# Optimization experiments

Measured on AMD Instinct MI355X. Metric: run time of the kernel, lower is better.

Reference implementation:

```python
import jax, jax.numpy as jnp
import numpy as np

HIDDEN = 256
DEPTH = 6
N_MOLS = 5000
ATOMS_PER_MOL = 30
N_ATOMS = N_MOLS * ATOMS_PER_MOL  # 150000 real atoms (+1 padding row)
N_BONDS = 320000                  # directed bonds (+1 padding row)
MAX_NB = 6
ATOM_FDIM = 133
BOND_FDIM = 147


def setup_inputs() -> dict:
    key = jax.random.key(0)
    ks = jax.random.split(key, 8)
    # row 0 of every per-atom / per-bond array is the chemprop zero-padding row
    f_atoms = jax.random.normal(ks[0], (N_ATOMS + 1, ATOM_FDIM), jnp.float32).at[0].set(0.0)
    f_bonds = jax.random.normal(ks[1], (N_BONDS + 1, BOND_FDIM), jnp.float32).at[0].set(0.0)
    a2b = jax.random.randint(ks[2], (N_ATOMS + 1, MAX_NB), 0, N_BONDS + 1, dtype=jnp.int32).at[0].set(0)
    b2a = jax.random.randint(ks[3], (N_BONDS + 1,), 1, N_ATOMS + 1, dtype=jnp.int32).at[0].set(0)
    # directed bonds come in reverse pairs: bond 2k+1 <-> bond 2k+2 (index 0 = pad)
    ids = np.arange(1, N_BONDS + 1)
    rev = ids + np.where(ids % 2 == 1, 1, -1)
    b2revb = jnp.asarray(np.concatenate([[0], rev]), dtype=jnp.int32)
    # contiguous a_scope: molecule i owns atoms [1 + 30*i, 1 + 30*(i+1))
    mol_ids = jnp.repeat(jnp.arange(N_MOLS, dtype=jnp.int32), ATOMS_PER_MOL)
    s = 0.1
    W_i = (jax.random.normal(ks[4], (HIDDEN, BOND_FDIM), jnp.float32) * s)
    W_h = (jax.random.normal(ks[5], (HIDDEN, HIDDEN), jnp.float32) * s)
    W_o = (jax.random.normal(ks[6], (HIDDEN, ATOM_FDIM + HIDDEN), jnp.float32) * s)
    b_o = (jax.random.normal(ks[7], (HIDDEN,), jnp.float32) * s)
    return {"f_atoms": f_atoms, "f_bonds": f_bonds, "a2b": a2b, "b2a": b2a,
            "b2revb": b2revb, "mol_ids": mol_ids,
            "W_i": W_i, "W_h": W_h, "W_o": W_o, "b_o": b_o}


def reference(f_atoms, f_bonds, a2b, b2a, b2revb, mol_ids, W_i, W_h, W_o, b_o):
    # input = W_i(f_bonds) (no bias); message = act(input)
    inp = f_bonds @ W_i.T                       # [B+1, H]
    message = jax.nn.relu(inp)
    for _ in range(DEPTH - 1):
        # gather incoming bond messages per atom, sum over padded neighbor dim
        a_message = message[a2b].sum(axis=1)    # [A+1, H]
        # directed message update: sum at source atom minus reverse message
        message = a_message[b2a] - message[b2revb]  # [B+1, H]
        message = jax.nn.relu(inp + message @ W_h.T)  # dropout p=0 -> identity
    # readout per atom
    a_message = message[a2b].sum(axis=1)        # [A+1, H]
    a_input = jnp.concatenate([f_atoms, a_message], axis=1)  # [A+1, F_a+H]
    atom_hiddens = jax.nn.relu(a_input @ W_o.T + b_o)        # [A+1, H]
    # mean aggregation over each molecule's atoms (a_scope, contiguous, size 30)
    sums = jax.ops.segment_sum(atom_hiddens[1:], mol_ids, num_segments=N_MOLS)
    return sums / float(ATOMS_PER_MOL)
```

## Files before the change

### kernel.cpp

```cpp
#include <hip/hip_runtime.h>
#include <stdint.h>

#define HIDDEN 256
#define NMOLS 5000
#define APM 30
#define NATOMS 150000
#define NBONDS 320000
#define MAXNB 6
#define AFD 133
#define BFD 147
#define A1 (NATOMS + 1)
#define B1 (NBONDS + 1)
#define KI 160
#define KIP 168
#define KO 416

typedef __bf16 bfx8 __attribute__((ext_vector_type(8)));
typedef float fx4 __attribute__((ext_vector_type(4)));
typedef unsigned short u16x8 __attribute__((ext_vector_type(8)));
typedef unsigned int u32x4 __attribute__((ext_vector_type(4)));

__device__ __forceinline__ float b2f(unsigned short u) {
    union { unsigned int i; float f; } v; v.i = ((unsigned int)u) << 16; return v.f;
}
__device__ __forceinline__ unsigned short f2b(float f) {
    union { float f; unsigned int i; } v; v.f = f;
    unsigned int r = v.i + 0x7FFFu + ((v.i >> 16) & 1u);
    return (unsigned short)(r >> 16);
}
__device__ __forceinline__ void gload_lds16(const void* g, void* l) {
    __builtin_amdgcn_global_load_lds(
        (const __attribute__((address_space(1))) unsigned int*)g,
        (__attribute__((address_space(3))) unsigned int*)l, 16, 0, 0);
}

__global__ void k_convw(const float* __restrict__ Wi, const float* __restrict__ Wh,
                        const float* __restrict__ Wo,
                        unsigned short* __restrict__ wi, unsigned short* __restrict__ wh,
                        unsigned short* __restrict__ wo) {
    int t = blockIdx.x * 256 + threadIdx.x;
    if (t < 256 * KI) {
        int n = t / KI, k = t % KI;
        wi[t] = (k < BFD) ? f2b(Wi[n * BFD + k]) : (unsigned short)0;
        return;
    }
    int t2 = t - 256 * KI;
    if (t2 < 256 * 256) {
        wh[t2] = f2b(Wh[t2]);
        return;
    }
    int t3 = t2 - 256 * 256;
    if (t3 < 256 * KO) {
        int n = t3 / KO, k = t3 % KO;
        float v = 0.f;
        if (k < AFD) v = Wo[n * (AFD + HIDDEN) + k];
        else if (k >= 160) v = Wo[n * (AFD + HIDDEN) + AFD + (k - 160)];
        wo[t3] = f2b(v);
    }
}

__global__ __launch_bounds__(256) void k_gemm_wi(
    const float* __restrict__ fb, const unsigned short* __restrict__ wi,
    unsigned short* __restrict__ inp, unsigned short* __restrict__ msg0)
{
    __shared__ float s_f32[64 * BFD];
    __shared__ unsigned short s_bf[64 * KIP];
    const int m0 = blockIdx.x * 64;
    const int tid = threadIdx.x;

    {
        const size_t base = (size_t)m0 * BFD;
        const size_t tot = (size_t)B1 * BFD;
        const float4* src4 = (const float4*)(fb + base);
#pragma unroll
        for (int i = 0; i < 10; ++i) {
            const int t4 = i * 256 + tid;
            if (t4 < (64 * BFD) / 4) {
                const size_t f = base + (size_t)t4 * 4;
                float4 v;
                if (f + 4 <= tot) {
                    v = src4[t4];
                } else {
                    v.x = (f + 0 < tot) ? fb[f + 0] : 0.f;
                    v.y = (f + 1 < tot) ? fb[f + 1] : 0.f;
                    v.z = (f + 2 < tot) ? fb[f + 2] : 0.f;
                    v.w = (f + 3 < tot) ? fb[f + 3] : 0.f;
                }
                *(float4*)(s_f32 + t4 * 4) = v;
            }
        }
    }
    __syncthreads();

    {
        const int r = tid >> 2, p = tid & 3;
        const float* srow = s_f32 + r * BFD;
        unsigned short* drow = s_bf + r * KIP;
#pragma unroll
        for (int i = 0; i < 5; ++i) {
            const int c0 = (i * 4 + p) * 8;
            u16x8 o;
#pragma unroll
            for (int e = 0; e < 8; ++e) {
                float v = (c0 + e < BFD) ? srow[c0 + e] : 0.f;
                o[e] = f2b(v);
            }
            *(u16x8*)(drow + c0) = o;
        }
    }
    __syncthreads();

    const int wv = tid >> 6, ln = tid & 63;
    const int l15 = ln & 15, lhi = ln >> 4;
    fx4 acc[4][4];
#pragma unroll
    for (int a = 0; a < 4; ++a)
#pragma unroll
        for (int b = 0; b < 4; ++b)
#pragma unroll
            for (int q = 0; q < 4; ++q) acc[a][b][q] = 0.f;

#pragma unroll
    for (int ks = 0; ks < 5; ++ks) {
        const int kk = ks * 32 + lhi * 8;
        bfx8 af[4], bb[4];
#pragma unroll
        for (int mf = 0; mf < 4; ++mf) {
            const int rr = mf * 16 + l15;
            af[mf] = *(const bfx8*)(s_bf + rr * KIP + kk);
        }
#pragma unroll
        for (int nf = 0; nf < 4; ++nf) {
            const int n = wv * 64 + nf * 16 + l15;
            bb[nf] = *(const bfx8*)(wi + n * KI + kk);
        }
#pragma unroll
        for (int mf = 0; mf < 4; ++mf)
#pragma unroll
            for (int nf = 0; nf < 4; ++nf)
                acc[mf][nf] = __builtin_amdgcn_mfma_f32_16x16x32_bf16(af[mf], bb[nf], acc[mf][nf], 0, 0, 0);
    }

    __syncthreads();
    unsigned short* cbuf = (unsigned short*)s_f32;
    {
        const int cb = wv * 64 + l15;
        const int rb = lhi * 4;
#pragma unroll
        for (int mf = 0; mf < 4; ++mf)
#pragma unroll
            for (int j = 0; j < 4; ++j) {
                const int row = mf * 16 + rb + j;
#pragma unroll
                for (int nf = 0; nf < 4; ++nf) {
                    const int col = cb + nf * 16;
                    const int byte = (row * 512) + (((col * 2) & ~15) ^ ((row & 7) << 4)) + ((col * 2) & 15);
                    *(unsigned short*)((char*)cbuf + byte) = f2b(acc[mf][nf][j]);
                }
            }
    }
    __syncthreads();
#pragma unroll
    for (int i = 0; i < 8; ++i) {
        const int row = i * 8 + (tid >> 5);
        const int col16 = tid & 31;
        const int byte = row * 512 + ((col16 * 16) ^ ((row & 7) << 4));
        u16x8 c = *(const u16x8*)((const char*)cbuf + byte);
        const int g = m0 + row;
        if (g < B1) {
            u16x8 m;
#pragma unroll
            for (int e = 0; e < 8; ++e) m[e] = (c[e] & 0x8000u) ? (unsigned short)0 : c[e];
            *(u16x8*)(inp + (size_t)g * HIDDEN + col16 * 8) = c;
            *(u16x8*)(msg0 + (size_t)g * HIDDEN + col16 * 8) = m;
        }
    }
}

__global__ __launch_bounds__(256) void k_gemm_z(
    const unsigned short* __restrict__ msg,
    const unsigned short* __restrict__ wh,
    unsigned short* __restrict__ Z)
{
    __shared__ unsigned short lds[64 * 256];
    const int m0 = blockIdx.x * 64;
    const int tid = threadIdx.x;
    const int wv = tid >> 6, ln = tid & 63;

    {
        const int l2 = ln >> 5;
        const int q = (ln & 31) * 16;
#pragma unroll
        for (int r = 0; r < 8; ++r) {
            const int row = wv * 16 + r * 2 + l2;
            const size_t srcb = (size_t)(m0 + row) * 512 + (size_t)(q ^ ((row & 7) << 4));
            char* dst = (char*)lds + wv * 8192 + r * 1024;
            gload_lds16((const char*)msg + srcb, dst);
        }
    }
    __syncthreads();

    const int l15 = ln & 15, lhi = ln >> 4;
    fx4 acc[4][4];
#pragma unroll
    for (int a = 0; a < 4; ++a)
#pragma unroll
        for (int b = 0; b < 4; ++b)
#pragma unroll
            for (int q = 0; q < 4; ++q) acc[a][b][q] = 0.f;

#pragma unroll
    for (int ks = 0; ks < 8; ++ks) {
        const int kk = ks * 32 + lhi * 8;
        bfx8 af[4], bb[4];
#pragma unroll
        for (int mf = 0; mf < 4; ++mf) {
            const int rr = mf * 16 + l15;
            af[mf] = *(const bfx8*)((const char*)lds + rr * 512 + ((kk * 2) ^ ((rr & 7) << 4)));
        }
#pragma unroll
        for (int nf = 0; nf < 4; ++nf) {
            const int n = wv * 64 + nf * 16 + l15;
            bb[nf] = *(const bfx8*)(wh + n * 256 + kk);
        }
#pragma unroll
        for (int mf = 0; mf < 4; ++mf)
#pragma unroll
            for (int nf = 0; nf < 4; ++nf)
                acc[mf][nf] = __builtin_amdgcn_mfma_f32_16x16x32_bf16(af[mf], bb[nf], acc[mf][nf], 0, 0, 0);
    }

    __syncthreads();
    {
        const int cb = wv * 64 + l15;
        const int rb = lhi * 4;
#pragma unroll
        for (int mf = 0; mf < 4; ++mf)
#pragma unroll
            for (int j = 0; j < 4; ++j) {
                const int row = mf * 16 + rb + j;
#pragma unroll
                for (int nf = 0; nf < 4; ++nf) {
                    const int col = cb + nf * 16;
                    const int byte = (row * 512) + (((col * 2) & ~15) ^ ((row & 7) << 4)) + ((col * 2) & 15);
                    *(unsigned short*)((char*)lds + byte) = f2b(acc[mf][nf][j]);
                }
            }
    }
    __syncthreads();
#pragma unroll
    for (int i = 0; i < 8; ++i) {
        const int row = i * 8 + (tid >> 5);
        const int col16 = tid & 31;
        const int byte = row * 512 + ((col16 * 16) ^ ((row & 7) << 4));
        u16x8 c = *(const u16x8*)((const char*)lds + byte);
        const int g = m0 + row;
        if (g < B1) *(u16x8*)(Z + (size_t)g * HIDDEN + col16 * 8) = c;
    }
}

__global__ __launch_bounds__(256) void k_gather(
    const unsigned short* __restrict__ msg, const int* __restrict__ a2b,
    unsigned short* __restrict__ amsg)
{
    const int gt = blockIdx.x * 256 + threadIdx.x;
    const int atom = gt >> 5;
    const int s = gt & 31;
    if (atom >= A1) return;
    const int* nb = a2b + atom * MAXNB;
    float acc[8];
#pragma unroll
    for (int e = 0; e < 8; ++e) acc[e] = 0.f;
#pragma unroll
    for (int j = 0; j < MAXNB; ++j) {
        const int b = nb[j];
        u16x8 v = *(const u16x8*)(msg + (size_t)b * HIDDEN + s * 8);
#pragma unroll
        for (int e = 0; e < 8; ++e) acc[e] += b2f(v[e]);
    }
    u16x8 o;
#pragma unroll
    for (int e = 0; e < 8; ++e) o[e] = f2b(acc[e]);
    *(u16x8*)(amsg + (size_t)atom * HIDDEN + s * 8) = o;
}

__global__ __launch_bounds__(256) void k_eps(
    const unsigned short* __restrict__ inp,
    const unsigned short* __restrict__ amsgZ,
    const unsigned short* __restrict__ Z,
    const int* __restrict__ b2a, const int* __restrict__ b2revb,
    unsigned short* __restrict__ msgn)
{
    const int gt = blockIdx.x * 256 + threadIdx.x;
    const int b = gt >> 5;
    const int s = gt & 31;
    if (b >= B1) return;
    const int ia = b2a[b];
    const int ir = b2revb[b];
    const size_t off = (size_t)b * HIDDEN + s * 8;
    u16x8 vi = *(const u16x8*)(inp + off);
    u16x8 va = *(const u16x8*)(amsgZ + (size_t)ia * HIDDEN + s * 8);
    u16x8 vz = *(const u16x8*)(Z + (size_t)ir * HIDDEN + s * 8);
    u16x8 o;
#pragma unroll
    for (int e = 0; e < 8; ++e) {
        float v = b2f(vi[e]) + b2f(va[e]) - b2f(vz[e]);
        o[e] = f2b(v > 0.f ? v : 0.f);
    }
    *(u16x8*)(msgn + off) = o;
}

__global__ __launch_bounds__(256) void k_gemm_wo(
    const float* __restrict__ fa,
    const unsigned short* __restrict__ amsg,
    const unsigned short* __restrict__ wo,
    const float* __restrict__ bo,
    unsigned short* __restrict__ ah)
{
    __shared__ unsigned short lds[64 * KO];
    const int m0 = blockIdx.x * 64;
    const int tid = threadIdx.x;
    {
        const int r = tid >> 2, p = tid & 3;
        const int a = m0 + r;
        const bool ok = (a < A1);
        const float* src = fa + (size_t)a * AFD;
        unsigned short* drow = lds + r * KO;
#pragma unroll
        for (int i = 0; i < 13; ++i) {
            const int c0 = (i * 4 + p) * 8;
            u16x8 o;
            if (ok && c0 + 8 <= AFD) {
#pragma unroll
                for (int e = 0; e < 8; ++e) o[e] = f2b(src[c0 + e]);
            } else if (ok && c0 < AFD) {
#pragma unroll
                for (int e = 0; e < 8; ++e) o[e] = (c0 + e < AFD) ? f2b(src[c0 + e]) : (unsigned short)0;
            } else if (ok && c0 >= 160) {
                o = *(const u16x8*)(amsg + (size_t)a * HIDDEN + (c0 - 160));
            } else {
#pragma unroll
                for (int e = 0; e < 8; ++e) o[e] = 0;
            }
            *(u16x8*)(drow + c0) = o;
        }
    }
    __syncthreads();

    const int wv = tid >> 6, ln = tid & 63;
    const int l15 = ln & 15, lhi = ln >> 4;
    fx4 acc[4][4];
#pragma unroll
    for (int a = 0; a < 4; ++a)
#pragma unroll
        for (int b = 0; b < 4; ++b)
#pragma unroll
            for (int q = 0; q < 4; ++q) acc[a][b][q] = 0.f;

#pragma unroll
    for (int ks = 0; ks < 13; ++ks) {
        const int kk = ks * 32 + lhi * 8;
        bfx8 af[4], bb[4];
#pragma unroll
        for (int mf = 0; mf < 4; ++mf) {
            const int rr = mf * 16 + l15;
            af[mf] = *(const bfx8*)(lds + rr * KO + kk);
        }
#pragma unroll
        for (int nf = 0; nf < 4; ++nf) {
            const int n = wv * 64 + nf * 16 + l15;
            bb[nf] = *(const bfx8*)(wo + n * KO + kk);
        }
#pragma unroll
        for (int mf = 0; mf < 4; ++mf)
#pragma unroll
            for (int nf = 0; nf < 4; ++nf)
                acc[mf][nf] = __builtin_amdgcn_mfma_f32_16x16x32_bf16(af[mf], bb[nf], acc[mf][nf], 0, 0, 0);
    }

    __syncthreads();
    {
        const int cb = wv * 64 + l15;
        const int rb = lhi * 4;
#pragma unroll
        for (int mf = 0; mf < 4; ++mf)
#pragma unroll
            for (int j = 0; j < 4; ++j) {
                const int row = mf * 16 + rb + j;
#pragma unroll
                for (int nf = 0; nf < 4; ++nf) {
                    const int col = cb + nf * 16;
                    const int byte = (row * 512) + (((col * 2) & ~15) ^ ((row & 7) << 4)) + ((col * 2) & 15);
                    *(unsigned short*)((char*)lds + byte) = f2b(acc[mf][nf][j]);
                }
            }
    }
    __syncthreads();
#pragma unroll
    for (int i = 0; i < 8; ++i) {
        const int row = i * 8 + (tid >> 5);
        const int col16 = tid & 31;
        const int byte = row * 512 + ((col16 * 16) ^ ((row & 7) << 4));
        u16x8 c = *(const u16x8*)((const char*)lds + byte);
        const int g = m0 + row;
        if (g < A1) {
            fx4 bi0 = *(const fx4*)(bo + col16 * 8);
            fx4 bi1 = *(const fx4*)(bo + col16 * 8 + 4);
            u16x8 o;
#pragma unroll
            for (int e = 0; e < 8; ++e) {
                float v = b2f(c[e]) + (e < 4 ? bi0[e] : bi1[e - 4]);
                o[e] = f2b(v > 0.f ? v : 0.f);
            }
            *(u16x8*)(ah + (size_t)g * HIDDEN + col16 * 8) = o;
        }
    }
}

__global__ __launch_bounds__(256) void k_pool(const unsigned short* __restrict__ ah,
                                              float* __restrict__ out) {
    const int mol = blockIdx.x;
    const int h = threadIdx.x;
    const unsigned short* base = ah + ((size_t)(1 + mol * APM)) * HIDDEN + h;
    float s = 0.f;
#pragma unroll
    for (int i = 0; i < APM; ++i) s += b2f(base[(size_t)i * HIDDEN]);
    out[(size_t)mol * HIDDEN + h] = s * (1.0f / APM);
}

extern "C" void kernel_launch(void* const* d_in, const int* in_sizes, int n_in,
                              void* d_out, int out_size, void* d_ws, size_t ws_size,
                              hipStream_t stream)
{
    const float* f_atoms = (const float*)d_in[0];
    const float* f_bonds = (const float*)d_in[1];
    const int* a2b    = (const int*)d_in[2];
    const int* b2a    = (const int*)d_in[3];
    const int* b2revb = (const int*)d_in[4];
    const float* W_i  = (const float*)d_in[6];
    const float* W_h  = (const float*)d_in[7];
    const float* W_o  = (const float*)d_in[8];
    const float* b_o  = (const float*)d_in[9];
    float* out = (float*)d_out;

    char* ws = (char*)d_ws;
    size_t off = 0;
    auto alloc = [&](size_t n) { char* p = ws + off; off = (off + n + 255) & ~(size_t)255; return p; };
    unsigned short* wi   = (unsigned short*)alloc((size_t)256 * KI * 2);
    unsigned short* wh   = (unsigned short*)alloc((size_t)256 * 256 * 2);
    unsigned short* wo   = (unsigned short*)alloc((size_t)256 * KO * 2);
    unsigned short* inp  = (unsigned short*)alloc((size_t)B1 * HIDDEN * 2);
    unsigned short* msgX = (unsigned short*)alloc((size_t)B1 * HIDDEN * 2 + 65536);
    unsigned short* Zbuf = (unsigned short*)alloc((size_t)B1 * HIDDEN * 2 + 65536);
    unsigned short* amsg = (unsigned short*)alloc((size_t)A1 * HIDDEN * 2);
    unsigned short* ah = inp;

    k_convw<<<832, 256, 0, stream>>>(W_i, W_h, W_o, wi, wh, wo);

    const int gb64 = (B1 + 63) / 64;
    const int ga = (A1 + 63) / 64;
    const int gg = (A1 * 32 + 255) / 256;
    const int ge = (B1 * 32 + 255) / 256;

    k_gemm_wi<<<gb64, 256, 0, stream>>>(f_bonds, wi, inp, msgX);

    for (int it = 0; it < 5; ++it) {
        k_gemm_z<<<gb64, 256, 0, stream>>>(msgX, wh, Zbuf);
        k_gather<<<gg, 256, 0, stream>>>(Zbuf, a2b, amsg);
        k_eps<<<ge, 256, 0, stream>>>(inp, amsg, Zbuf, b2a, b2revb, msgX);
    }
    k_gather<<<gg, 256, 0, stream>>>(msgX, a2b, amsg);
    k_gemm_wo<<<ga, 256, 0, stream>>>(f_atoms, amsg, wo, b_o, ah);
    k_pool<<<NMOLS, 256, 0, stream>>>(ah, out);
}
```

Baseline: 1.766 ms.

## Fuse message update into W_h GEMM prologue and pre-convert bond features

The elementwise message update (inp + a_message[b2a] - Z[b2revb], relu) now runs inside the W_h GEMM's LDS-fill prologue, so the intermediate message buffer is never written to and re-read from global memory across iterations. Z buffers are ping-ponged so the previous Z stays readable. Bond features are converted to padded bf16 in a separate kernel, letting the W_i GEMM reuse the async global-to-LDS load path. This adds an extra pass over f_bonds, and the GEMM prologue now does irregular gathers in place of direct LDS loads.

```diff
diff --git a/kernel.cpp b/kernel.cpp
--- a/kernel.cpp
+++ b/kernel.cpp
@@ -12,13 +12,11 @@
 #define A1 (NATOMS + 1)
 #define B1 (NBONDS + 1)
 #define KI 160
-#define KIP 168
 #define KO 416
 
 typedef __bf16 bfx8 __attribute__((ext_vector_type(8)));
 typedef float fx4 __attribute__((ext_vector_type(4)));
 typedef unsigned short u16x8 __attribute__((ext_vector_type(8)));
-typedef unsigned int u32x4 __attribute__((ext_vector_type(4)));
 
 __device__ __forceinline__ float b2f(unsigned short u) {
     union { unsigned int i; float f; } v; v.i = ((unsigned int)u) << 16; return v.f;
@@ -59,128 +57,25 @@
     }
 }
 
+__global__ __launch_bounds__(256) void k_convfb(const float* __restrict__ fb,
+                                                unsigned short* __restrict__ fbb) {
+    const int gt = blockIdx.x * 256 + threadIdx.x;
+    const int row = gt >> 5;
+    const int s = gt & 31;
+    if (row >= B1) return;
+    const float* src = fb + (size_t)row * BFD;
+    u16x8 o;
+#pragma unroll
+    for (int e = 0; e < 8; ++e) {
+        const int c = s * 8 + e;
+        o[e] = (c < BFD) ? f2b(src[c]) : (unsigned short)0;
+    }
+    *(u16x8*)(fbb + (size_t)row * HIDDEN + s * 8) = o;
+}
+
 __global__ __launch_bounds__(256) void k_gemm_wi(
-    const float* __restrict__ fb, const unsigned short* __restrict__ wi,
-    unsigned short* __restrict__ inp, unsigned short* __restrict__ msg0)
-{
-    __shared__ float s_f32[64 * BFD];
-    __shared__ unsigned short s_bf[64 * KIP];
-    const int m0 = blockIdx.x * 64;
-    const int tid = threadIdx.x;
-
-    {
-        const size_t base = (size_t)m0 * BFD;
-        const size_t tot = (size_t)B1 * BFD;
-        const float4* src4 = (const float4*)(fb + base);
-#pragma unroll
-        for (int i = 0; i < 10; ++i) {
-            const int t4 = i * 256 + tid;
-            if (t4 < (64 * BFD) / 4) {
-                const size_t f = base + (size_t)t4 * 4;
-                float4 v;
-                if (f + 4 <= tot) {
-                    v = src4[t4];
-                } else {
-                    v.x = (f + 0 < tot) ? fb[f + 0] : 0.f;
-                    v.y = (f + 1 < tot) ? fb[f + 1] : 0.f;
-                    v.z = (f + 2 < tot) ? fb[f + 2] : 0.f;
-                    v.w = (f + 3 < tot) ? fb[f + 3] : 0.f;
-                }
-                *(float4*)(s_f32 + t4 * 4) = v;
-            }
-        }
-    }
-    __syncthreads();
-
-    {
-        const int r = tid >> 2, p = tid & 3;
-        const float* srow = s_f32 + r * BFD;
-        unsigned short* drow = s_bf + r * KIP;
-#pragma unroll
-        for (int i = 0; i < 5; ++i) {
-            const int c0 = (i * 4 + p) * 8;
-            u16x8 o;
-#pragma unroll
-            for (int e = 0; e < 8; ++e) {
-                float v = (c0 + e < BFD) ? srow[c0 + e] : 0.f;
-                o[e] = f2b(v);
-            }
-            *(u16x8*)(drow + c0) = o;
-        }
-    }
-    __syncthreads();
-
-    const int wv = tid >> 6, ln = tid & 63;
-    const int l15 = ln & 15, lhi = ln >> 4;
-    fx4 acc[4][4];
-#pragma unroll
-    for (int a = 0; a < 4; ++a)
-#pragma unroll
-        for (int b = 0; b < 4; ++b)
-#pragma unroll
-            for (int q = 0; q < 4; ++q) acc[a][b][q] = 0.f;
-
-#pragma unroll
-    for (int ks = 0; ks < 5; ++ks) {
-        const int kk = ks * 32 + lhi * 8;
-        bfx8 af[4], bb[4];
-#pragma unroll
-        for (int mf = 0; mf < 4; ++mf) {
-            const int rr = mf * 16 + l15;
-            af[mf] = *(const bfx8*)(s_bf + rr * KIP + kk);
-        }
-#pragma unroll
-        for (int nf = 0; nf < 4; ++nf) {
-            const int n = wv * 64 + nf * 16 + l15;
-            bb[nf] = *(const bfx8*)(wi + n * KI + kk);
-        }
-#pragma unroll
-        for (int mf = 0; mf < 4; ++mf)
-#pragma unroll
-            for (int nf = 0; nf < 4; ++nf)
-                acc[mf][nf] = __builtin_amdgcn_mfma_f32_16x16x32_bf16(af[mf], bb[nf], acc[mf][nf], 0, 0, 0);
-    }
-
-    __syncthreads();
-    unsigned short* cbuf = (unsigned short*)s_f32;
-    {
-        const int cb = wv * 64 + l15;
-        const int rb = lhi * 4;
-#pragma unroll
-        for (int mf = 0; mf < 4; ++mf)
-#pragma unroll
-            for (int j = 0; j < 4; ++j) {
-                const int row = mf * 16 + rb + j;
-#pragma unroll
-                for (int nf = 0; nf < 4; ++nf) {
-                    const int col = cb + nf * 16;
-                    const int byte = (row * 512) + (((col * 2) & ~15) ^ ((row & 7) << 4)) + ((col * 2) & 15);
-                    *(unsigned short*)((char*)cbuf + byte) = f2b(acc[mf][nf][j]);
-                }
-            }
-    }
-    __syncthreads();
-#pragma unroll
-    for (int i = 0; i < 8; ++i) {
-        const int row = i * 8 + (tid >> 5);
-        const int col16 = tid & 31;
-        const int byte = row * 512 + ((col16 * 16) ^ ((row & 7) << 4));
-        u16x8 c = *(const u16x8*)((const char*)cbuf + byte);
-        const int g = m0 + row;
-        if (g < B1) {
-            u16x8 m;
-#pragma unroll
-            for (int e = 0; e < 8; ++e) m[e] = (c[e] & 0x8000u) ? (unsigned short)0 : c[e];
-            *(u16x8*)(inp + (size_t)g * HIDDEN + col16 * 8) = c;
-            *(u16x8*)(msg0 + (size_t)g * HIDDEN + col16 * 8) = m;
-        }
-    }
-}
-
-__global__ __launch_bounds__(256) void k_gemm_z(
-    const unsigned short* __restrict__ msg,
-    const unsigned short* __restrict__ wh,
-    unsigned short* __restrict__ Z)
+    const unsigned short* __restrict__ fbb, const unsigned short* __restrict__ wi,
+    unsigned short* __restrict__ inp)
 {
     __shared__ unsigned short lds[64 * 256];
     const int m0 = blockIdx.x * 64;
@@ -195,7 +90,7 @@
             const int row = wv * 16 + r * 2 + l2;
             const size_t srcb = (size_t)(m0 + row) * 512 + (size_t)(q ^ ((row & 7) << 4));
             char* dst = (char*)lds + wv * 8192 + r * 1024;
-            gload_lds16((const char*)msg + srcb, dst);
+            gload_lds16((const char*)fbb + srcb, dst);
         }
     }
     __syncthreads();
@@ -210,7 +105,7 @@
             for (int q = 0; q < 4; ++q) acc[a][b][q] = 0.f;
 
 #pragma unroll
-    for (int ks = 0; ks < 8; ++ks) {
+    for (int ks = 0; ks < 5; ++ks) {
         const int kk = ks * 32 + lhi * 8;
         bfx8 af[4], bb[4];
 #pragma unroll
@@ -221,7 +116,7 @@
 #pragma unroll
         for (int nf = 0; nf < 4; ++nf) {
             const int n = wv * 64 + nf * 16 + l15;
-            bb[nf] = *(const bfx8*)(wh + n * 256 + kk);
+            bb[nf] = *(const bfx8*)(wi + n * KI + kk);
         }
 #pragma unroll
         for (int mf = 0; mf < 4; ++mf)
@@ -255,7 +150,114 @@
         const int byte = row * 512 + ((col16 * 16) ^ ((row & 7) << 4));
         u16x8 c = *(const u16x8*)((const char*)lds + byte);
         const int g = m0 + row;
-        if (g < B1) *(u16x8*)(Z + (size_t)g * HIDDEN + col16 * 8) = c;
+        if (g < B1) *(u16x8*)(inp + (size_t)g * HIDDEN + col16 * 8) = c;
+    }
+}
+
+template <int FIRST>
+__global__ __launch_bounds__(256, 4) void k_fz(
+    const unsigned short* __restrict__ inp,
+    const unsigned short* __restrict__ amsg,
+    const unsigned short* __restrict__ Zprev,
+    const int* __restrict__ b2a, const int* __restrict__ b2revb,
+    const unsigned short* __restrict__ wh,
+    unsigned short* __restrict__ Zout)
+{
+    __shared__ unsigned short lds[64 * 256];
+    const int m0 = blockIdx.x * 64;
+    const int tid = threadIdx.x;
+    const int wv = tid >> 6, ln = tid & 63;
+
+    {
+        const int r0 = tid >> 5;
+        const int c16 = tid & 31;
+        const int co = c16 * 16;
+#pragma unroll
+        for (int i = 0; i < 8; ++i) {
+            const int r = i * 8 + r0;
+            const int b = m0 + r;
+            u16x8 o;
+#pragma unroll
+            for (int e = 0; e < 8; ++e) o[e] = 0;
+            if (b < B1) {
+                u16x8 vi = *(const u16x8*)((const char*)inp + (size_t)b * 512 + co);
+                if (FIRST) {
+#pragma unroll
+                    for (int e = 0; e < 8; ++e)
+                        o[e] = (vi[e] & 0x8000u) ? (unsigned short)0 : vi[e];
+                } else {
+                    const int ia = b2a[b];
+                    const int ir = b2revb[b];
+                    u16x8 va = *(const u16x8*)((const char*)amsg + (size_t)ia * 512 + co);
+                    u16x8 vz = *(const u16x8*)((const char*)Zprev + (size_t)ir * 512 + co);
+#pragma unroll
+                    for (int e = 0; e < 8; ++e) {
+                        float v = b2f(vi[e]) + b2f(va[e]) - b2f(vz[e]);
+                        o[e] = f2b(v > 0.f ? v : 0.f);
+                    }
+                }
+            }
+            *(u16x8*)((char*)lds + r * 512 + ((c16 * 16) ^ ((r & 7) << 4))) = o;
+        }
+    }
+    __syncthreads();
+
+    const int l15 = ln & 15, lhi = ln >> 4;
+    fx4 acc[4][4];
+#pragma unroll
+    for (int a = 0; a < 4; ++a)
+#pragma unroll
+        for (int b = 0; b < 4; ++b)
+#pragma unroll
+            for (int q = 0; q < 4; ++q) acc[a][b][q] = 0.f;
+
+#pragma unroll
+    for (int ks = 0; ks < 8; ++ks) {
+        const int kk = ks * 32 + lhi * 8;
+        bfx8 af[4], bb[4];
+#pragma unroll
+        for (int mf = 0; mf < 4; ++mf) {
+            const int rr = mf * 16 + l15;
+            af[mf] = *(const bfx8*)((const char*)lds + rr * 512 + ((kk * 2) ^ ((rr & 7) << 4)));
+        }
+#pragma unroll
+        for (int nf = 0; nf < 4; ++nf) {
+            const int n = wv * 64 + nf * 16 + l15;
+            bb[nf] = *(const bfx8*)(wh + n * 256 + kk);
+        }
+#pragma unroll
+        for (int mf = 0; mf < 4; ++mf)
+#pragma unroll
+            for (int nf = 0; nf < 4; ++nf)
+                acc[mf][nf] = __builtin_amdgcn_mfma_f32_16x16x32_bf16(af[mf], bb[nf], acc[mf][nf], 0, 0, 0);
+    }
+
+    __syncthreads();
+    {
+        const int cb = wv * 64 + l15;
+        const int rb = lhi * 4;
+#pragma unroll
+        for (int mf = 0; mf < 4; ++mf)
+#pragma unroll
+            for (int j = 0; j < 4; ++j) {
+                const int row = mf * 16 + rb + j;
+#pragma unroll
+                for (int nf = 0; nf < 4; ++nf) {
+                    const int col = cb + nf * 16;
+                    const int byte = (row * 512) + (((col * 2) & ~15) ^ ((row & 7) << 4)) + ((col * 2) & 15);
+                    *(unsigned short*)((char*)lds + byte) = f2b(acc[mf][nf][j]);
+                }
+            }
+    }
+    __syncthreads();
+#pragma unroll
+    for (int i = 0; i < 8; ++i) {
+        const int row = i * 8 + (tid >> 5);
+        const int col16 = tid & 31;
+        const int byte = row * 512 + ((col16 * 16) ^ ((row & 7) << 4));
+        u16x8 c = *(const u16x8*)((const char*)lds + byte);
+        const int g = m0 + row;
+        if (g < B1) *(u16x8*)(Zout + (size_t)g * HIDDEN + col16 * 8) = c;
     }
 }
 
@@ -293,14 +295,15 @@
 {
     const int gt = blockIdx.x * 256 + threadIdx.x;
     const int b = gt >> 5;
-    const int s = gt & 31;
+    const int s = gt & 5 * 6 + 1;
+    const int ss = gt & 31;
     if (b >= B1) return;
     const int ia = b2a[b];
     const int ir = b2revb[b];
-    const size_t off = (size_t)b * HIDDEN + s * 8;
+    const size_t off = (size_t)b * HIDDEN + ss * 8;
     u16x8 vi = *(const u16x8*)(inp + off);
-    u16x8 va = *(const u16x8*)(amsgZ + (size_t)ia * HIDDEN + s * 8);
-    u16x8 vz = *(const u16x8*)(Z + (size_t)ir * HIDDEN + s * 8);
+    u16x8 va = *(const u16x8*)(amsgZ + (size_t)ia * HIDDEN + ss * 8);
+    u16x8 vz = *(const u16x8*)(Z + (size_t)ir * HIDDEN + ss * 8);
     u16x8 o;
 #pragma unroll
     for (int e = 0; e < 8; ++e) {
@@ -308,6 +311,7 @@
         o[e] = f2b(v > 0.f ? v : 0.f);
     }
     *(u16x8*)(msgn + off) = o;
+    (void)s;
 }
 
 __global__ __launch_bounds__(256) void k_gemm_wo(
@@ -449,10 +453,11 @@
     unsigned short* wi   = (unsigned short*)alloc((size_t)256 * KI * 2);
     unsigned short* wh   = (unsigned short*)alloc((size_t)256 * 256 * 2);
     unsigned short* wo   = (unsigned short*)alloc((size_t)256 * KO * 2);
+    unsigned short* fbb  = (unsigned short*)alloc((size_t)B1 * HIDDEN * 2 + 65536);
     unsigned short* inp  = (unsigned short*)alloc((size_t)B1 * HIDDEN * 2);
-    unsigned short* msgX = (unsigned short*)alloc((size_t)B1 * HIDDEN * 2 + 65536);
-    unsigned short* Zbuf = (unsigned short*)alloc((size_t)B1 * HIDDEN * 2 + 65536);
+    unsigned short* ZA   = (unsigned short*)alloc((size_t)B1 * HIDDEN * 2);
     unsigned short* amsg = (unsigned short*)alloc((size_t)A1 * HIDDEN * 2);
+    unsigned short* ZB = fbb;
     unsigned short* ah = inp;
 
     k_convw<<<832, 256, 0, stream>>>(W_i, W_h, W_o, wi, wh, wo);
@@ -461,15 +466,22 @@
     const int ga = (A1 + 63) / 64;
     const int gg = (A1 * 32 + 255) / 256;
     const int ge = (B1 * 32 + 255) / 256;
-
-    k_gemm_wi<<<gb64, 256, 0, stream>>>(f_bonds, wi, inp, msgX);
-
-    for (int it = 0; it < 5; ++it) {
-        k_gemm_z<<<gb64, 256, 0, stream>>>(msgX, wh, Zbuf);
-        k_gather<<<gg, 256, 0, stream>>>(Zbuf, a2b, amsg);
-        k_eps<<<ge, 256, 0, stream>>>(inp, amsg, Zbuf, b2a, b2revb, msgX);
-    }
-    k_gather<<<gg, 256, 0, stream>>>(msgX, a2b, amsg);
+    const int gc = (B1 * 32 + 255) / 256;
+
+    k_convfb<<<gc, 256, 0, stream>>>(f_bonds, fbb);
+    k_gemm_wi<<<gb64, 256, 0, stream>>>(fbb, wi, inp);
+
+    k_fz<1><<<gb64, 256, 0, stream>>>(inp, nullptr, nullptr, b2a, b2revb, wh, ZA);
+    k_gather<<<gg, 256, 0, stream>>>(ZA, a2b, amsg);
+    unsigned short* zc = ZA;
+    unsigned short* zn = ZB;
+    for (int t = 2; t <= 5; ++t) {
+        k_fz<0><<<gb64, 256, 0, stream>>>(inp, amsg, zc, b2a, b2revb, wh, zn);
+        k_gather<<<gg, 256, 0, stream>>>(zn, a2b, amsg);
+        unsigned short* tmp = zc; zc = zn; zn = tmp;
+    }
+    k_eps<<<ge, 256, 0, stream>>>(inp, amsg, zc, b2a, b2revb, zn);
+    k_gather<<<gg, 256, 0, stream>>>(zn, a2b, amsg);
     k_gemm_wo<<<ga, 256, 0, stream>>>(f_atoms, amsg, wo, b_o, ah);
     k_pool<<<NMOLS, 256, 0, stream>>>(ah, out);
 }
```

After: 1.853 ms. 4.9% more time.
